# Kernel optimization log

Measured on AMD Instinct MI355X. Metric: run time of the kernel, lower is better.

## Reference

```python
import jax, jax.numpy as jnp
import numpy as np

N_NODES = 100000
N_EDGES = 3200000
IN_DIM, HD_DIM, OUT_DIM = 512, 256, 128


def spmm(edge_row, edge_col, edge_val, x):
    # y[i] = sum_{e: row[e]=i} val[e] * x[col[e]]  -- sparse adj @ dense x
    msgs = edge_val[:, None] * x[edge_col]          # [E, D]
    return jax.ops.segment_sum(msgs, edge_row, num_segments=N_NODES)


def setup_inputs() -> dict:
    key = jax.random.key(0)
    k1, k2, k3, k4, k5, k6, k7, k8 = jax.random.split(key, 8)
    x = jax.random.normal(k1, (N_NODES, IN_DIM), dtype=jnp.float32)
    edge_row = jax.random.randint(k2, (N_EDGES,), 0, N_NODES, dtype=jnp.int64)
    edge_col = jax.random.randint(k3, (N_EDGES,), 0, N_NODES, dtype=jnp.int64)
    edge_val = jax.random.uniform(k4, (N_EDGES,), dtype=jnp.float32)
    s0 = 1.0 / np.sqrt(IN_DIM)
    s1 = 1.0 / np.sqrt(HD_DIM)
    W0 = jax.random.uniform(k5, (IN_DIM, HD_DIM), dtype=jnp.float32, minval=-s0, maxval=s0)
    b0 = jax.random.uniform(k6, (HD_DIM,), dtype=jnp.float32, minval=-s0, maxval=s0)
    W1 = jax.random.uniform(k7, (HD_DIM, OUT_DIM), dtype=jnp.float32, minval=-s1, maxval=s1)
    b1 = jax.random.uniform(k8, (OUT_DIM,), dtype=jnp.float32, minval=-s1, maxval=s1)
    return {"x": x, "edge_row": edge_row, "edge_col": edge_col, "edge_val": edge_val,
            "W0": W0, "b0": b0, "W1": W1, "b1": b1}


def reference(x, edge_row, edge_col, edge_val, W0, b0, W1, b1):
    # eval mode: dropout is identity
    h = x @ W0 + b0                                  # li0: [N, HD]
    h = spmm(edge_row, edge_col, edge_val, h)        # adj @ h
    h = spmm(edge_row, edge_col, edge_val, h)        # adj @ (adj @ h)
    return jax.nn.relu(h) @ W1 + b1                  # li1(relu(.)): [N, OUT]
```

## Files before the change

kernel.cpp:

```cpp
#include <hip/hip_runtime.h>

#define N_NODES 100000
#define N_EDGES 3200000
#define IN_DIM  512
#define HD_DIM  256
#define OUT_DIM 128

#define NBINS  1563
#define BINCAP 2560
#define SORT_IT 10
#define EPT    16
#define EPB    (256 * EPT)

typedef short   short8  __attribute__((ext_vector_type(8)));
typedef unsigned short ushort8 __attribute__((ext_vector_type(8)));
typedef float   floatx4 __attribute__((ext_vector_type(4)));

__device__ __forceinline__ unsigned short f2bf(float f) {
    unsigned int u = __float_as_uint(f);
    u += 0x7fffu + ((u >> 16) & 1u);
    return (unsigned short)(u >> 16);
}

__device__ __forceinline__ unsigned f2bf_pk(float lo, float hi) {
    unsigned r;
    asm("v_cvt_pk_bf16_f32 %0, %1, %2" : "=v"(r) : "v"(lo), "v"(hi));
    return r;
}


__global__ __launch_bounds__(256) void bin_scatter(const int* __restrict__ erow,
                                                   const int* __restrict__ ecol,
                                                   const float* __restrict__ eval,
                                                   int* __restrict__ gcnt,
                                                   uint2* __restrict__ binned, int E) {
    __shared__ int hist[NBINS];
    __shared__ int cur[NBINS];
    __shared__ int gbase[NBINS];
    const int t = threadIdx.x;
    for (int i = t; i < NBINS; i += 256) hist[i] = 0;
    __syncthreads();

    long base = (long)blockIdx.x * EPB + t * EPT;
    int rows[EPT];
    const bool valid = base < E;
    if (valid) {
        const int4* p = (const int4*)(erow + base);
#pragma unroll
        for (int v = 0; v < 4; v++) {
            int4 r = p[v];
            rows[4 * v + 0] = r.x; rows[4 * v + 1] = r.y;
            rows[4 * v + 2] = r.z; rows[4 * v + 3] = r.w;
        }
#pragma unroll
        for (int u = 0; u < EPT; u++) atomicAdd(&hist[rows[u] >> 6], 1);
    }
    __syncthreads();

    for (int i = t; i < NBINS; i += 256) {
        int h = hist[i];
        cur[i] = 0;
        gbase[i] = h ? (i * BINCAP + atomicAdd(&gcnt[i], h)) : 0;
    }
    __syncthreads();

    if (valid) {
        const int4*   pc = (const int4*)(ecol + base);
        const float4* pv = (const float4*)(eval + base);
#pragma unroll
        for (int v = 0; v < 4; v++) {
            int4 c4 = pc[v];
            float4 v4 = pv[v];
            int   cs[4] = {c4.x, c4.y, c4.z, c4.w};
            float vs[4] = {v4.x, v4.y, v4.z, v4.w};
#pragma unroll
            for (int u = 0; u < 4; u++) {
                int r = rows[4 * v + u];
                int bin = r >> 6;
                int lofs = atomicAdd(&cur[bin], 1);
                binned[gbase[bin] + lofs] =
                    make_uint2(((unsigned)(r & 63) << 26) | (unsigned)cs[u],
                               __float_as_uint(vs[u]));
            }
        }
    }
}


__global__ __launch_bounds__(256) void spmm_sort(const int* __restrict__ gcnt,
                                                 const uint2* __restrict__ binned,
                                                 int* __restrict__ rowptr,
                                                 int* __restrict__ binend,
                                                 uint2* __restrict__ csr,
                                                 const unsigned short* __restrict__ Hin,
                                                 unsigned short* __restrict__ Hout) {
    __shared__ uint2 ssort[BINCAP];
    __shared__ int hist[64];
    __shared__ int sd[64];
    __shared__ int cur[64];
    const int t = threadIdx.x;
    const int b = blockIdx.x;
    int n = gcnt[b];
    if (n > BINCAP) n = BINCAP;
    const int s = b * BINCAP;
    const int rows_base = b << 6;

    if (t < 64) hist[t] = 0;
    __syncthreads();

    uint2 ereg[SORT_IT];
#pragma unroll
    for (int it = 0; it < SORT_IT; it++) {
        int i = it * 256 + t;
        if (i < n) {
            ereg[it] = binned[s + i];
            atomicAdd(&hist[ereg[it].x >> 26], 1);
        }
    }
    __syncthreads();

    if (t < 64) sd[t] = hist[t];
    __syncthreads();
#pragma unroll
    for (int off = 1; off < 64; off <<= 1) {
        int add = 0;
        if (t < 64 && t >= off) add = sd[t - off];
        __syncthreads();
        if (t < 64) sd[t] += add;
        __syncthreads();
    }
    if (t < 64) {
        int ex = sd[t] - hist[t];
        cur[t] = ex;
        int r = rows_base + t;
        if (r <= N_NODES) rowptr[r] = s + ex;
    }
    if (t == 0) binend[b] = s + n;
    __syncthreads();

#pragma unroll
    for (int it = 0; it < SORT_IT; it++) {
        int i = it * 256 + t;
        if (i < n) {
            int rl = ereg[it].x >> 26;
            int p = atomicAdd(&cur[rl], 1);
            ssort[p] = make_uint2(ereg[it].x & 0x03FFFFFFu, ereg[it].y);
        }
    }
    __syncthreads();

    for (int i = t; i < n; i += 256) csr[s + i] = ssort[i];

    const int wave = t >> 6;
    const int lane = t & 63;
    const uint2* __restrict__ Hv = (const uint2*)Hin;
    for (int rl = wave; rl < 64; rl += 4) {
        const int r = rows_base + rl;
        if (r >= N_NODES) break;
        const int ks = sd[rl] - hist[rl];
        const int ke = sd[rl];
        float a0 = 0.f, a1 = 0.f, a2 = 0.f, a3 = 0.f;
        for (int j0 = ks; j0 < ke; j0 += 8) {
            int m = ke - j0;
            if (m > 8) m = 8;
            unsigned c[8];
            float    v[8];
            uint2    h[8];
#pragma unroll
            for (int u = 0; u < 8; u++) {
                if (u < m) {
                    uint2 e = ssort[j0 + u];
                    c[u] = e.x;
                    v[u] = __uint_as_float(e.y);
                } else { c[u] = 0u; v[u] = 0.f; }
            }
#pragma unroll
            for (int u = 0; u < 8; u++) h[u] = Hv[(c[u] << 6) + lane];
#pragma unroll
            for (int u = 0; u < 8; u++) {
                a0 += v[u] * __uint_as_float(h[u].x << 16);
                a1 += v[u] * __uint_as_float(h[u].x & 0xffff0000u);
                a2 += v[u] * __uint_as_float(h[u].y << 16);
                a3 += v[u] * __uint_as_float(h[u].y & 0xffff0000u);
            }
        }
        unsigned long long o = (unsigned long long)((unsigned)f2bf(a0) | ((unsigned)f2bf(a1) << 16))
                             | ((unsigned long long)((unsigned)f2bf(a2) | ((unsigned)f2bf(a3) << 16)) << 32);
        __builtin_nontemporal_store(o, (unsigned long long*)Hout + (((unsigned)r << 6) + lane));
    }
}


__global__ void transpose_w(const float* __restrict__ W0, unsigned short* __restrict__ W0T,
                            const float* __restrict__ W1, unsigned short* __restrict__ W1T) {
    int idx = blockIdx.x * blockDim.x + threadIdx.x;
    if (idx < IN_DIM * HD_DIM) {
        int k = idx / HD_DIM, n = idx - k * HD_DIM;
        W0T[n * IN_DIM + k] = f2bf(W0[idx]);
    } else {
        int j = idx - IN_DIM * HD_DIM;
        if (j < HD_DIM * OUT_DIM) {
            int k = j / OUT_DIM, n = j - k * OUT_DIM;
            W1T[n * HD_DIM + k] = f2bf(W1[j]);
        }
    }
}


template <bool A_FP32, bool RELU_A, bool OUT_BF16, int BN>
__global__ __launch_bounds__(256, 2) void gemm_mfma(const void* __restrict__ Av,
                                                    const unsigned short* __restrict__ BT,
                                                    const float* __restrict__ bias,
                                                    void* __restrict__ Cv,
                                                    int M, int N, int K) {
    constexpr int NJ = BN / 32;
    __shared__ unsigned short As[128 * 40];
    __shared__ unsigned short Bs[BN * 40];
    const int tid  = threadIdx.x;
    const int lane = tid & 63;
    const int wv   = tid >> 6;
    const int wm   = (wv >> 1) * 64;
    const int wn   = (wv & 1) * (BN / 2);
    const int mrow = lane & 15;
    const int q    = lane >> 4;
    const int bm   = blockIdx.x * 128;
    const int bn   = blockIdx.y * BN;

    floatx4 acc[4][NJ] = {};

    const int srow = tid >> 1;
    const int skh  = (tid & 1) * 16;

    for (int k0 = 0; k0 < K; k0 += 32) {
        {
            const int grow = bm + srow;
            if (A_FP32) {
                uint4 w0, w1;
                if (grow < M) {
                    const float* A = (const float*)Av;
                    const float4* p = (const float4*)&A[(long)grow * K + k0 + skh];
                    float4 f;
                    f = p[0]; w0.x = f2bf_pk(f.x, f.y); w0.y = f2bf_pk(f.z, f.w);
                    f = p[1]; w0.z = f2bf_pk(f.x, f.y); w0.w = f2bf_pk(f.z, f.w);
                    f = p[2]; w1.x = f2bf_pk(f.x, f.y); w1.y = f2bf_pk(f.z, f.w);
                    f = p[3]; w1.z = f2bf_pk(f.x, f.y); w1.w = f2bf_pk(f.z, f.w);
                } else {
                    w0 = make_uint4(0, 0, 0, 0);
                    w1 = make_uint4(0, 0, 0, 0);
                }
                *(uint4*)&As[srow * 40 + skh]     = w0;
                *(uint4*)&As[srow * 40 + skh + 8] = w1;
            } else {
                unsigned short tmp[16];
                const unsigned short* A = (const unsigned short*)Av;
                if (grow < M) {
                    const ushort8* p = (const ushort8*)&A[(long)grow * K + k0 + skh];
                    ushort8 u0 = p[0], u1 = p[1];
#pragma unroll
                    for (int v = 0; v < 8; v++) { tmp[v] = u0[v]; tmp[8 + v] = u1[v]; }
                    if (RELU_A) {
#pragma unroll
                        for (int v = 0; v < 16; v++)
                            if (tmp[v] & 0x8000u) tmp[v] = 0;
                    }
                } else {
#pragma unroll
                    for (int v = 0; v < 16; v++) tmp[v] = 0;
                }
                ushort8* dst = (ushort8*)&As[srow * 40 + skh];
                ushort8 w0, w1;
#pragma unroll
                for (int v = 0; v < 8; v++) { w0[v] = tmp[v]; w1[v] = tmp[8 + v]; }
                dst[0] = w0;
                dst[1] = w1;
            }
        }
        if (BN == 128) {
            const int gn = bn + srow;
            const ushort8* p = (const ushort8*)&BT[(long)gn * K + k0 + skh];
            ushort8* dst = (ushort8*)&Bs[srow * 40 + skh];
            dst[0] = p[0];
            dst[1] = p[1];
        } else {
            const int gn = bn + tid;
            const ushort8* p = (const ushort8*)&BT[(long)gn * K + k0];
            ushort8* dst = (ushort8*)&Bs[tid * 40];
            dst[0] = p[0];
            dst[1] = p[1];
            dst[2] = p[2];
            dst[3] = p[3];
        }
        __syncthreads();

        short8 af[4], bf[NJ];
#pragma unroll
        for (int i = 0; i < 4; i++)
            af[i] = *(const short8*)&As[(wm + i * 16 + mrow) * 40 + q * 8];
#pragma unroll
        for (int j = 0; j < NJ; j++)
            bf[j] = *(const short8*)&Bs[(wn + j * 16 + mrow) * 40 + q * 8];
#pragma unroll
        for (int i = 0; i < 4; i++)
#pragma unroll
            for (int j = 0; j < NJ; j++)
                acc[i][j] = __builtin_amdgcn_mfma_f32_16x16x32_bf16(af[i], bf[j], acc[i][j], 0, 0, 0);
        __syncthreads();
    }

#pragma unroll
    for (int i = 0; i < 4; i++) {
#pragma unroll
        for (int r = 0; r < 4; r++) {
            const int row = bm + wm + i * 16 + q * 4 + r;
            if (row < M) {
#pragma unroll
                for (int j = 0; j < NJ; j++) {
                    const int col = bn + wn + j * 16 + mrow;
                    float v = acc[i][j][r] + bias[col];
                    if (OUT_BF16)
                        ((unsigned short*)Cv)[(long)row * N + col] = f2bf(v);
                    else
                        ((float*)Cv)[(long)row * N + col] = v;
                }
            }
        }
    }
}


__global__ __launch_bounds__(256) void spmm_bf16(const int* __restrict__ rowptr,
                                                 const int* __restrict__ binend,
                                                 const uint2* __restrict__ edges,
                                                 const unsigned short* __restrict__ Hin,
                                                 unsigned short* __restrict__ Hout) {
    const int wave = threadIdx.x >> 6;
    const int lane = threadIdx.x & 63;
    const int r = blockIdx.x * 4 + wave;
    if (r >= N_NODES) return;
    const int s = rowptr[r];
    const int e = ((r & 63) == 63) ? binend[r >> 6] : rowptr[r + 1];
    const uint2* __restrict__ Hv = (const uint2*)Hin;
    float a0 = 0.f, a1 = 0.f, a2 = 0.f, a3 = 0.f;

    for (int base = s; base < e; base += 64) {
        int idx = base + lane;
        uint2 ev = make_uint2(0u, 0u);
        if (idx < e) {
            unsigned long long raw =
                __builtin_nontemporal_load((const unsigned long long*)edges + idx);
            ev.x = (unsigned)raw;
            ev.y = (unsigned)(raw >> 32);
        }
        int cnt = e - base;
        if (cnt > 64) cnt = 64;
        for (int j0 = 0; j0 < cnt; j0 += 8) {
            uint2 h[8];
            float v[8];
#pragma unroll
            for (int u = 0; u < 8; u++) {
                int   c = __shfl((int)ev.x, j0 + u);
                v[u]    = __uint_as_float((unsigned)__shfl((int)ev.y, j0 + u));
                h[u]    = Hv[((unsigned)c << 6) + lane];
            }
#pragma unroll
            for (int u = 0; u < 8; u++) {
                a0 += v[u] * __uint_as_float(h[u].x << 16);
                a1 += v[u] * __uint_as_float(h[u].x & 0xffff0000u);
                a2 += v[u] * __uint_as_float(h[u].y << 16);
                a3 += v[u] * __uint_as_float(h[u].y & 0xffff0000u);
            }
        }
    }
    unsigned long long o = (unsigned long long)((unsigned)f2bf(a0) | ((unsigned)f2bf(a1) << 16))
                         | ((unsigned long long)((unsigned)f2bf(a2) | ((unsigned)f2bf(a3) << 16)) << 32);
    __builtin_nontemporal_store(o, (unsigned long long*)Hout + (((unsigned)r << 6) + lane));
}


extern "C" void kernel_launch(void* const* d_in, const int* in_sizes, int n_in,
                              void* d_out, int out_size, void* d_ws, size_t ws_size,
                              hipStream_t stream) {
    const float* x    = (const float*)d_in[0];
    const int*   erow = (const int*)d_in[1];
    const int*   ecol = (const int*)d_in[2];
    const float* eval = (const float*)d_in[3];
    const float* W0   = (const float*)d_in[4];
    const float* b0   = (const float*)d_in[5];
    const float* W1   = (const float*)d_in[6];
    const float* b1   = (const float*)d_in[7];
    float* out = (float*)d_out;

    char* ws = (char*)d_ws;
    size_t off = 0;
    auto alloc = [&](size_t bytes) {
        void* p = ws + off;
        off += (bytes + 255) & ~(size_t)255;
        return p;
    };
    int*            rowptr   = (int*)alloc((N_NODES + 1) * sizeof(int));
    int*            gcnt     = (int*)alloc(NBINS * sizeof(int));
    int*            binend   = (int*)alloc(NBINS * sizeof(int));
    uint2*          binned   = (uint2*)alloc((size_t)NBINS * BINCAP * sizeof(uint2));
    uint2*          csr      = (uint2*)alloc((size_t)NBINS * BINCAP * sizeof(uint2));
    unsigned short* W0T      = (unsigned short*)alloc((size_t)IN_DIM * HD_DIM * sizeof(unsigned short));
    unsigned short* W1T      = (unsigned short*)alloc((size_t)HD_DIM * OUT_DIM * sizeof(unsigned short));
    unsigned short* Ha       = (unsigned short*)alloc((size_t)N_NODES * HD_DIM * sizeof(unsigned short));
    unsigned short* Hb       = (unsigned short*)alloc((size_t)N_NODES * HD_DIM * sizeof(unsigned short));

    const int nblk = (N_EDGES + EPB - 1) / EPB;

    hipMemsetAsync(gcnt, 0, NBINS * sizeof(int), stream);
    bin_scatter<<<nblk, 256, 0, stream>>>(erow, ecol, eval, gcnt, binned, N_EDGES);

    transpose_w<<<(IN_DIM * HD_DIM + HD_DIM * OUT_DIM + 255) / 256, 256, 0, stream>>>(
        W0, W0T, W1, W1T);

    gemm_mfma<true, false, true, 256><<<dim3((N_NODES + 127) / 128, HD_DIM / 256), 256, 0, stream>>>(
        x, W0T, b0, Ha, N_NODES, HD_DIM, IN_DIM);

    spmm_sort<<<NBINS, 256, 0, stream>>>(gcnt, binned, rowptr, binend, csr, Ha, Hb);

    spmm_bf16<<<(N_NODES + 3) / 4, 256, 0, stream>>>(rowptr, binend, csr, Hb, Ha);

    gemm_mfma<false, true, false, 128><<<dim3((N_NODES + 127) / 128, OUT_DIM / 128), 256, 0, stream>>>(
        Ha, W1T, b1, out, N_NODES, OUT_DIM, HD_DIM);
}
```

Measured before the change: 894.6 us.

## Sort edges within each bin by column segment then row for gather locality

The SpMM bin kernel now sorts each bin's edges by a composite key of column segment (col>>13) and local row. Waves sweep the 13 column segments in order and keep 16 row accumulators in registers, so concurrently running blocks gather from a narrower window of H and get better L2 reuse. The separate CSR write-out and the second spmm_bf16 kernel are gone. Both SpMM passes now run the same kernel on the binned data, repeating the in-LDS sort. The cost is a 1024-entry LDS scan, more register pressure from 16 float4 accumulators, and a redundant sort in the second pass.

```diff
diff --git a/kernel.cpp b/kernel.cpp
--- a/kernel.cpp
+++ b/kernel.cpp
@@ -9,6 +9,8 @@
 #define NBINS  1563
 #define BINCAP 2560
 #define SORT_IT 10
+#define NSEG   13
+#define NKEYS  (NSEG * 64)
 #define EPT    16
 #define EPB    (256 * EPT)
 
@@ -87,25 +89,20 @@
 }
 
 
-__global__ __launch_bounds__(256) void spmm_sort(const int* __restrict__ gcnt,
-                                                 const uint2* __restrict__ binned,
-                                                 int* __restrict__ rowptr,
-                                                 int* __restrict__ binend,
-                                                 uint2* __restrict__ csr,
-                                                 const unsigned short* __restrict__ Hin,
-                                                 unsigned short* __restrict__ Hout) {
+__global__ __launch_bounds__(256) void spmm_seg(const int* __restrict__ gcnt,
+                                                const uint2* __restrict__ binned,
+                                                const unsigned short* __restrict__ Hin,
+                                                unsigned short* __restrict__ Hout) {
     __shared__ uint2 ssort[BINCAP];
-    __shared__ int hist[64];
-    __shared__ int sd[64];
-    __shared__ int cur[64];
+    __shared__ int sd[1024];
+    __shared__ int cur[NKEYS];
     const int t = threadIdx.x;
     const int b = blockIdx.x;
     int n = gcnt[b];
     if (n > BINCAP) n = BINCAP;
-    const int s = b * BINCAP;
-    const int rows_base = b << 6;
-
-    if (t < 64) hist[t] = 0;
+    const long s = (long)b * BINCAP;
+
+    sd[t] = 0; sd[t + 256] = 0; sd[t + 512] = 0; sd[t + 768] = 0;
     __syncthreads();
 
     uint2 ereg[SORT_IT];
@@ -113,80 +110,85 @@
     for (int it = 0; it < SORT_IT; it++) {
         int i = it * 256 + t;
         if (i < n) {
-            ereg[it] = binned[s + i];
-            atomicAdd(&hist[ereg[it].x >> 26], 1);
-        }
-    }
-    __syncthreads();
-
-    if (t < 64) sd[t] = hist[t];
-    __syncthreads();
-#pragma unroll
-    for (int off = 1; off < 64; off <<= 1) {
-        int add = 0;
-        if (t < 64 && t >= off) add = sd[t - off];
+            unsigned long long raw =
+                __builtin_nontemporal_load((const unsigned long long*)binned + (s + i));
+            ereg[it].x = (unsigned)raw;
+            ereg[it].y = (unsigned)(raw >> 32);
+            unsigned key = ((ereg[it].x & 0x03FFFFFFu) >> 13) * 64u + (ereg[it].x >> 26);
+            atomicAdd(&sd[key], 1);
+        }
+    }
+    __syncthreads();
+
+    for (int off = 1; off < 1024; off <<= 1) {
+        int a0 = (t >= off) ? sd[t - off] : 0;
+        int a1 = (t + 256 >= off) ? sd[t + 256 - off] : 0;
+        int a2 = (t + 512 >= off) ? sd[t + 512 - off] : 0;
+        int a3 = (t + 768 >= off) ? sd[t + 768 - off] : 0;
         __syncthreads();
-        if (t < 64) sd[t] += add;
+        sd[t] += a0; sd[t + 256] += a1; sd[t + 512] += a2; sd[t + 768] += a3;
         __syncthreads();
     }
-    if (t < 64) {
-        int ex = sd[t] - hist[t];
-        cur[t] = ex;
-        int r = rows_base + t;
-        if (r <= N_NODES) rowptr[r] = s + ex;
-    }
-    if (t == 0) binend[b] = s + n;
+
+    for (int k = t; k < NKEYS; k += 256) cur[k] = (k == 0) ? 0 : sd[k - 1];
     __syncthreads();
 
 #pragma unroll
     for (int it = 0; it < SORT_IT; it++) {
         int i = it * 256 + t;
         if (i < n) {
-            int rl = ereg[it].x >> 26;
-            int p = atomicAdd(&cur[rl], 1);
-            ssort[p] = make_uint2(ereg[it].x & 0x03FFFFFFu, ereg[it].y);
-        }
-    }
-    __syncthreads();
-
-    for (int i = t; i < n; i += 256) csr[s + i] = ssort[i];
+            unsigned key = ((ereg[it].x & 0x03FFFFFFu) >> 13) * 64u + (ereg[it].x >> 26);
+            int p = atomicAdd(&cur[key], 1);
+            ssort[p] = ereg[it];
+        }
+    }
+    __syncthreads();
 
     const int wave = t >> 6;
     const int lane = t & 63;
     const uint2* __restrict__ Hv = (const uint2*)Hin;
-    for (int rl = wave; rl < 64; rl += 4) {
-        const int r = rows_base + rl;
-        if (r >= N_NODES) break;
-        const int ks = sd[rl] - hist[rl];
-        const int ke = sd[rl];
-        float a0 = 0.f, a1 = 0.f, a2 = 0.f, a3 = 0.f;
-        for (int j0 = ks; j0 < ke; j0 += 8) {
-            int m = ke - j0;
-            if (m > 8) m = 8;
-            unsigned c[8];
-            float    v[8];
-            uint2    h[8];
-#pragma unroll
-            for (int u = 0; u < 8; u++) {
-                if (u < m) {
-                    uint2 e = ssort[j0 + u];
-                    c[u] = e.x;
-                    v[u] = __uint_as_float(e.y);
-                } else { c[u] = 0u; v[u] = 0.f; }
+    floatx4 acc[16] = {};
+
+    for (int sg = 0; sg < NSEG; sg++) {
+#pragma unroll
+        for (int i = 0; i < 16; i++) {
+            const int key = sg * 64 + wave * 16 + i;
+            int ks = (key == 0) ? 0 : sd[key - 1];
+            int ke = sd[key];
+            for (int j0 = ks; j0 < ke; j0 += 4) {
+                int m = ke - j0;
+                if (m > 4) m = 4;
+                uint2 h[4];
+                float v[4];
+#pragma unroll
+                for (int u = 0; u < 4; u++) {
+                    if (u < m) {
+                        uint2 e = ssort[j0 + u];
+                        v[u] = __uint_as_float(e.y);
+                        h[u] = Hv[((e.x & 0x03FFFFFFu) << 6) + lane];
+                    } else { v[u] = 0.f; h[u] = make_uint2(0u, 0u); }
+                }
+#pragma unroll
+                for (int u = 0; u < 4; u++) {
+                    float vu = v[u];
+                    acc[i][0] += vu * __uint_as_float(h[u].x << 16);
+                    acc[i][1] += vu * __uint_as_float(h[u].x & 0xffff0000u);
+                    acc[i][2] += vu * __uint_as_float(h[u].y << 16);
+                    acc[i][3] += vu * __uint_as_float(h[u].y & 0xffff0000u);
+                }
             }
-#pragma unroll
-            for (int u = 0; u < 8; u++) h[u] = Hv[(c[u] << 6) + lane];
-#pragma unroll
-            for (int u = 0; u < 8; u++) {
-                a0 += v[u] * __uint_as_float(h[u].x << 16);
-                a1 += v[u] * __uint_as_float(h[u].x & 0xffff0000u);
-                a2 += v[u] * __uint_as_float(h[u].y << 16);
-                a3 += v[u] * __uint_as_float(h[u].y & 0xffff0000u);
-            }
-        }
-        unsigned long long o = (unsigned long long)((unsigned)f2bf(a0) | ((unsigned)f2bf(a1) << 16))
-                             | ((unsigned long long)((unsigned)f2bf(a2) | ((unsigned)f2bf(a3) << 16)) << 32);
-        __builtin_nontemporal_store(o, (unsigned long long*)Hout + (((unsigned)r << 6) + lane));
+        }
+    }
+
+#pragma unroll
+    for (int i = 0; i < 16; i++) {
+        const int row = (b << 6) + wave * 16 + i;
+        if (row < N_NODES) {
+            unsigned long long o =
+                (unsigned long long)((unsigned)f2bf(acc[i][0]) | ((unsigned)f2bf(acc[i][1]) << 16))
+              | ((unsigned long long)((unsigned)f2bf(acc[i][2]) | ((unsigned)f2bf(acc[i][3]) << 16)) << 32);
+            __builtin_nontemporal_store(o, (unsigned long long*)Hout + (((unsigned)row << 6) + lane));
+        }
     }
 }
 
@@ -328,55 +330,6 @@
 }
 
 
-__global__ __launch_bounds__(256) void spmm_bf16(const int* __restrict__ rowptr,
-                                                 const int* __restrict__ binend,
-                                                 const uint2* __restrict__ edges,
-                                                 const unsigned short* __restrict__ Hin,
-                                                 unsigned short* __restrict__ Hout) {
-    const int wave = threadIdx.x >> 6;
-    const int lane = threadIdx.x & 63;
-    const int r = blockIdx.x * 4 + wave;
-    if (r >= N_NODES) return;
-    const int s = rowptr[r];
-    const int e = ((r & 63) == 63) ? binend[r >> 6] : rowptr[r + 1];
-    const uint2* __restrict__ Hv = (const uint2*)Hin;
-    float a0 = 0.f, a1 = 0.f, a2 = 0.f, a3 = 0.f;
-
-    for (int base = s; base < e; base += 64) {
-        int idx = base + lane;
-        uint2 ev = make_uint2(0u, 0u);
-        if (idx < e) {
-            unsigned long long raw =
-                __builtin_nontemporal_load((const unsigned long long*)edges + idx);
-            ev.x = (unsigned)raw;
-            ev.y = (unsigned)(raw >> 32);
-        }
-        int cnt = e - base;
-        if (cnt > 64) cnt = 64;
-        for (int j0 = 0; j0 < cnt; j0 += 8) {
-            uint2 h[8];
-            float v[8];
-#pragma unroll
-            for (int u = 0; u < 8; u++) {
-                int   c = __shfl((int)ev.x, j0 + u);
-                v[u]    = __uint_as_float((unsigned)__shfl((int)ev.y, j0 + u));
-                h[u]    = Hv[((unsigned)c << 6) + lane];
-            }
-#pragma unroll
-            for (int u = 0; u < 8; u++) {
-                a0 += v[u] * __uint_as_float(h[u].x << 16);
-                a1 += v[u] * __uint_as_float(h[u].x & 0xffff0000u);
-                a2 += v[u] * __uint_as_float(h[u].y << 16);
-                a3 += v[u] * __uint_as_float(h[u].y & 0xffff0000u);
-            }
-        }
-    }
-    unsigned long long o = (unsigned long long)((unsigned)f2bf(a0) | ((unsigned)f2bf(a1) << 16))
-                         | ((unsigned long long)((unsigned)f2bf(a2) | ((unsigned)f2bf(a3) << 16)) << 32);
-    __builtin_nontemporal_store(o, (unsigned long long*)Hout + (((unsigned)r << 6) + lane));
-}
-
-
 extern "C" void kernel_launch(void* const* d_in, const int* in_sizes, int n_in,
                               void* d_out, int out_size, void* d_ws, size_t ws_size,
                               hipStream_t stream) {
@@ -397,11 +350,8 @@
         off += (bytes + 255) & ~(size_t)255;
         return p;
     };
-    int*            rowptr   = (int*)alloc((N_NODES + 1) * sizeof(int));
     int*            gcnt     = (int*)alloc(NBINS * sizeof(int));
-    int*            binend   = (int*)alloc(NBINS * sizeof(int));
     uint2*          binned   = (uint2*)alloc((size_t)NBINS * BINCAP * sizeof(uint2));
-    uint2*          csr      = (uint2*)alloc((size_t)NBINS * BINCAP * sizeof(uint2));
     unsigned short* W0T      = (unsigned short*)alloc((size_t)IN_DIM * HD_DIM * sizeof(unsigned short));
     unsigned short* W1T      = (unsigned short*)alloc((size_t)HD_DIM * OUT_DIM * sizeof(unsigned short));
     unsigned short* Ha       = (unsigned short*)alloc((size_t)N_NODES * HD_DIM * sizeof(unsigned short));
@@ -418,9 +368,8 @@
     gemm_mfma<true, false, true, 256><<<dim3((N_NODES + 127) / 128, HD_DIM / 256), 256, 0, stream>>>(
         x, W0T, b0, Ha, N_NODES, HD_DIM, IN_DIM);
 
-    spmm_sort<<<NBINS, 256, 0, stream>>>(gcnt, binned, rowptr, binend, csr, Ha, Hb);
-
-    spmm_bf16<<<(N_NODES + 3) / 4, 256, 0, stream>>>(rowptr, binend, csr, Hb, Ha);
+    spmm_seg<<<NBINS, 256, 0, stream>>>(gcnt, binned, Ha, Hb);
+    spmm_seg<<<NBINS, 256, 0, stream>>>(gcnt, binned, Hb, Ha);
 
     gemm_mfma<false, true, false, 128><<<dim3((N_NODES + 127) / 128, OUT_DIM / 128), 256, 0, stream>>>(
         Ha, W1T, b1, out, N_NODES, OUT_DIM, HD_DIM);
```

Measured after the change: 997.7 us. +11.5%, slower.

## Stage bin scatter in shared memory and widen bins to 256 rows

Applied to the files above, without the earlier changes.

The bin scatter kernel now prefix-sums its local histogram and stages edges sorted by bin in shared memory, then writes them to global memory contiguously, so scattered 8-byte stores become mostly coalesced runs. Bins grow from 64 to 256 rows (391 bins, capacity 9216), and the fused sort+first-SpMM kernel moves to 512 threads with 32 rows per wave. Fewer, larger bins cut global atomics and make scatter runs longer, but they raise shared memory per block (about 72KB of sort buffer, plus roughly 50KB of staging in the scatter kernel) and lower the number of blocks for the fused kernel. Any bin that overflows its capacity now has its excess edges dropped.

```diff
diff --git a/kernel.cpp b/kernel.cpp
--- a/kernel.cpp
+++ b/kernel.cpp
@@ -6,9 +6,9 @@
 #define HD_DIM  256
 #define OUT_DIM 128
 
-#define NBINS  1563
-#define BINCAP 2560
-#define SORT_IT 10
+#define NBINS  391
+#define BINCAP 9216
+#define SORT_IT 18
 #define EPT    16
 #define EPB    (256 * EPT)
 
@@ -35,8 +35,13 @@
                                                    int* __restrict__ gcnt,
                                                    uint2* __restrict__ binned, int E) {
     __shared__ int hist[NBINS];
+    __shared__ int sd[512];
+    __shared__ int lbase[NBINS];
+    __shared__ int gbase[NBINS];
     __shared__ int cur[NBINS];
-    __shared__ int gbase[NBINS];
+    __shared__ unsigned short sbin[EPB];
+    __shared__ uint2 sedge[EPB];
+
     const int t = threadIdx.x;
     for (int i = t; i < NBINS; i += 256) hist[i] = 0;
     __syncthreads();
@@ -53,13 +58,27 @@
             rows[4 * v + 2] = r.z; rows[4 * v + 3] = r.w;
         }
 #pragma unroll
-        for (int u = 0; u < EPT; u++) atomicAdd(&hist[rows[u] >> 6], 1);
-    }
-    __syncthreads();
+        for (int u = 0; u < EPT; u++) atomicAdd(&hist[rows[u] >> 8], 1);
+    }
+    __syncthreads();
+
+    sd[t]       = (t < NBINS) ? hist[t] : 0;
+    sd[t + 256] = (t + 256 < NBINS) ? hist[t + 256] : 0;
+    __syncthreads();
+    for (int off = 1; off < 512; off <<= 1) {
+        int a0 = (t >= off) ? sd[t - off] : 0;
+        int a1 = (t + 256 >= off) ? sd[t + 256 - off] : 0;
+        __syncthreads();
+        sd[t] += a0;
+        sd[t + 256] += a1;
+        __syncthreads();
+    }
 
     for (int i = t; i < NBINS; i += 256) {
-        int h = hist[i];
-        cur[i] = 0;
+        int h  = hist[i];
+        int lb = sd[i] - h;
+        lbase[i] = lb;
+        cur[i]   = lb;
         gbase[i] = h ? (i * BINCAP + atomicAdd(&gcnt[i], h)) : 0;
     }
     __syncthreads();
@@ -76,63 +95,71 @@
 #pragma unroll
             for (int u = 0; u < 4; u++) {
                 int r = rows[4 * v + u];
-                int bin = r >> 6;
-                int lofs = atomicAdd(&cur[bin], 1);
-                binned[gbase[bin] + lofs] =
-                    make_uint2(((unsigned)(r & 63) << 26) | (unsigned)cs[u],
-                               __float_as_uint(vs[u]));
-            }
-        }
-    }
-}
-
-
-__global__ __launch_bounds__(256) void spmm_sort(const int* __restrict__ gcnt,
-                                                 const uint2* __restrict__ binned,
-                                                 int* __restrict__ rowptr,
-                                                 int* __restrict__ binend,
-                                                 uint2* __restrict__ csr,
-                                                 const unsigned short* __restrict__ Hin,
-                                                 unsigned short* __restrict__ Hout) {
+                int bin = r >> 8;
+                int lpos = atomicAdd(&cur[bin], 1);
+                sedge[lpos] = make_uint2(((unsigned)(r & 255) << 20) | (unsigned)cs[u],
+                                         __float_as_uint(vs[u]));
+                sbin[lpos] = (unsigned short)bin;
+            }
+        }
+    }
+    __syncthreads();
+
+    const int ns = sd[NBINS - 1];
+    for (int i = t; i < ns; i += 256) {
+        int bin = sbin[i];
+        int gpos = gbase[bin] + (i - lbase[bin]);
+        if (gpos < (bin + 1) * BINCAP)
+            binned[gpos] = sedge[i];
+    }
+}
+
+
+__global__ __launch_bounds__(512) void spmm_fuse1(const int* __restrict__ gcnt,
+                                                  const uint2* __restrict__ binned,
+                                                  int* __restrict__ rowptr,
+                                                  int* __restrict__ binend,
+                                                  uint2* __restrict__ csr,
+                                                  const unsigned short* __restrict__ Hin,
+                                                  unsigned short* __restrict__ Hout) {
     __shared__ uint2 ssort[BINCAP];
-    __shared__ int hist[64];
-    __shared__ int sd[64];
-    __shared__ int cur[64];
+    __shared__ int hist[256];
+    __shared__ int sd[256];
+    __shared__ int cur[256];
     const int t = threadIdx.x;
     const int b = blockIdx.x;
     int n = gcnt[b];
     if (n > BINCAP) n = BINCAP;
     const int s = b * BINCAP;
-    const int rows_base = b << 6;
-
-    if (t < 64) hist[t] = 0;
+
+    if (t < 256) hist[t] = 0;
     __syncthreads();
 
     uint2 ereg[SORT_IT];
 #pragma unroll
     for (int it = 0; it < SORT_IT; it++) {
-        int i = it * 256 + t;
+        int i = it * 512 + t;
         if (i < n) {
             ereg[it] = binned[s + i];
-            atomicAdd(&hist[ereg[it].x >> 26], 1);
-        }
-    }
-    __syncthreads();
-
-    if (t < 64) sd[t] = hist[t];
-    __syncthreads();
-#pragma unroll
-    for (int off = 1; off < 64; off <<= 1) {
+            atomicAdd(&hist[ereg[it].x >> 20], 1);
+        }
+    }
+    __syncthreads();
+
+    int v = 0;
+    if (t < 256) { v = hist[t]; sd[t] = v; }
+    __syncthreads();
+    for (int off = 1; off < 256; off <<= 1) {
         int add = 0;
-        if (t < 64 && t >= off) add = sd[t - off];
-        __syncthreads();
-        if (t < 64) sd[t] += add;
-        __syncthreads();
-    }
-    if (t < 64) {
-        int ex = sd[t] - hist[t];
+        if (t < 256 && t >= off) add = sd[t - off];
+        __syncthreads();
+        if (t < 256) sd[t] += add;
+        __syncthreads();
+    }
+    if (t < 256) {
+        int ex = sd[t] - v;
         cur[t] = ex;
-        int r = rows_base + t;
+        int r = (b << 8) + t;
         if (r <= N_NODES) rowptr[r] = s + ex;
     }
     if (t == 0) binend[b] = s + n;
@@ -140,48 +167,47 @@
 
 #pragma unroll
     for (int it = 0; it < SORT_IT; it++) {
-        int i = it * 256 + t;
+        int i = it * 512 + t;
         if (i < n) {
-            int rl = ereg[it].x >> 26;
+            int rl = ereg[it].x >> 20;
             int p = atomicAdd(&cur[rl], 1);
-            ssort[p] = make_uint2(ereg[it].x & 0x03FFFFFFu, ereg[it].y);
-        }
-    }
-    __syncthreads();
-
-    for (int i = t; i < n; i += 256) csr[s + i] = ssort[i];
+            ssort[p] = make_uint2(ereg[it].x & 0xFFFFFu, ereg[it].y);
+        }
+    }
+    __syncthreads();
+
+    for (int i = t; i < n; i += 512) csr[s + i] = ssort[i];
 
     const int wave = t >> 6;
     const int lane = t & 63;
     const uint2* __restrict__ Hv = (const uint2*)Hin;
-    for (int rl = wave; rl < 64; rl += 4) {
-        const int r = rows_base + rl;
+    for (int q = 0; q < 32; q++) {
+        const int rl = wave * 32 + q;
+        const int r = (b << 8) + rl;
         if (r >= N_NODES) break;
-        const int ks = sd[rl] - hist[rl];
         const int ke = sd[rl];
+        const int ks = ke - hist[rl];
         float a0 = 0.f, a1 = 0.f, a2 = 0.f, a3 = 0.f;
         for (int j0 = ks; j0 < ke; j0 += 8) {
             int m = ke - j0;
             if (m > 8) m = 8;
-            unsigned c[8];
-            float    v[8];
-            uint2    h[8];
+            uint2 h[8];
+            float vv[8];
 #pragma unroll
             for (int u = 0; u < 8; u++) {
                 if (u < m) {
                     uint2 e = ssort[j0 + u];
-                    c[u] = e.x;
-                    v[u] = __uint_as_float(e.y);
-                } else { c[u] = 0u; v[u] = 0.f; }
-            }
-#pragma unroll
-            for (int u = 0; u < 8; u++) h[u] = Hv[(c[u] << 6) + lane];
+                    vv[u] = __uint_as_float(e.y);
+                    h[u]  = Hv[((unsigned)e.x << 6) + lane];
+                } else { vv[u] = 0.f; h[u] = make_uint2(0u, 0u); }
+            }
 #pragma unroll
             for (int u = 0; u < 8; u++) {
-                a0 += v[u] * __uint_as_float(h[u].x << 16);
-                a1 += v[u] * __uint_as_float(h[u].x & 0xffff0000u);
-                a2 += v[u] * __uint_as_float(h[u].y << 16);
-                a3 += v[u] * __uint_as_float(h[u].y & 0xffff0000u);
+                float vu = vv[u];
+                a0 += vu * __uint_as_float(h[u].x << 16);
+                a1 += vu * __uint_as_float(h[u].x & 0xffff0000u);
+                a2 += vu * __uint_as_float(h[u].y << 16);
+                a3 += vu * __uint_as_float(h[u].y & 0xffff0000u);
             }
         }
         unsigned long long o = (unsigned long long)((unsigned)f2bf(a0) | ((unsigned)f2bf(a1) << 16))
@@ -338,7 +364,7 @@
     const int r = blockIdx.x * 4 + wave;
     if (r >= N_NODES) return;
     const int s = rowptr[r];
-    const int e = ((r & 63) == 63) ? binend[r >> 6] : rowptr[r + 1];
+    const int e = ((r & 255) == 255) ? binend[r >> 8] : rowptr[r + 1];
     const uint2* __restrict__ Hv = (const uint2*)Hin;
     float a0 = 0.f, a1 = 0.f, a2 = 0.f, a3 = 0.f;
 
@@ -418,7 +444,7 @@
     gemm_mfma<true, false, true, 256><<<dim3((N_NODES + 127) / 128, HD_DIM / 256), 256, 0, stream>>>(
         x, W0T, b0, Ha, N_NODES, HD_DIM, IN_DIM);
 
-    spmm_sort<<<NBINS, 256, 0, stream>>>(gcnt, binned, rowptr, binend, csr, Ha, Hb);
+    spmm_fuse1<<<NBINS, 512, 0, stream>>>(gcnt, binned, rowptr, binend, csr, Ha, Hb);
 
     spmm_bf16<<<(N_NODES + 3) / 4, 256, 0, stream>>>(rowptr, binend, csr, Hb, Ha);
 
```

After: 872.0 us. 2.5% less time.
